# Optimization experiments

Measured on AMD Instinct MI355X. Metric: run time of the kernel, lower is better.

## Reference

```python
import jax, jax.numpy as jnp
import numpy as np

B, L, D = 2, 4096, 2048
H = 8
DK = D // H   # head qk dim = 256
DV = D // H   # head v dim = 256
KCONV = 4
BT = 64       # chunk size
EPS = 1e-5


def setup_inputs() -> dict:
    key = jax.random.key(0)
    ks = jax.random.split(key, 10)
    s = 0.02  # xavier-ish init scale (gain 2**-2.5)
    return {
        "hidden_states": jax.random.normal(ks[0], (B, L, D), jnp.float32),
        "Wq": jax.random.normal(ks[1], (D, D), jnp.float32) * s,
        "Wk": jax.random.normal(ks[2], (D, D), jnp.float32) * s,
        "Wv": jax.random.normal(ks[3], (D, D), jnp.float32) * s,
        "Wb": jax.random.normal(ks[4], (H, D), jnp.float32) * s,
        "conv_q": jax.random.normal(ks[5], (D, KCONV), jnp.float32) * 0.5,
        "conv_k": jax.random.normal(ks[6], (D, KCONV), jnp.float32) * 0.5,
        "conv_v": jax.random.normal(ks[7], (D, KCONV), jnp.float32) * 0.5,
        "g_norm": jnp.ones((DV,), jnp.float32),
        "Wo": jax.random.normal(ks[8], (D, D), jnp.float32) * s,
    }


def _causal_conv_silu(x, w):
    # depthwise causal conv1d (ShortConvolution), x: [B,L,C], w: [C,K]; silu activation
    K = w.shape[1]
    xp = jnp.pad(x, ((0, 0), (K - 1, 0), (0, 0)))
    Lx = x.shape[1]
    y = xp[:, 0:Lx, :] * w[:, 0]
    for j in range(1, K):
        y = y + xp[:, j:j + Lx, :] * w[:, j]
    return jax.nn.silu(y)


def _l2norm(x):
    return x * jax.lax.rsqrt(jnp.sum(x * x, -1, keepdims=True) + 1e-6)


def _chunk_delta_rule(q, k, v, beta):
    # q,k: [B,H,L,DK], v: [B,H,L,DV], beta: [B,H,L]
    b, h, Lq, dk = q.shape
    dv = v.shape[-1]
    nc = Lq // BT
    q = q * (dk ** -0.5)
    kb = k * beta[..., None]
    vb = v * beta[..., None]
    ch = lambda x: x.reshape(b, h, nc, BT, x.shape[-1])
    qc, kc, kbc, vbc = ch(q), ch(k), ch(kb), ch(vb)
    tri_s = jnp.tril(jnp.ones((BT, BT), bool), -1)  # strictly lower
    tri = jnp.tril(jnp.ones((BT, BT), bool))        # lower incl diag
    # M = strict_lower(K_beta K^T); T = (I+M)^{-1} via unit-lower triangular solve
    M = jnp.where(tri_s, jnp.einsum('bhntd,bhnsd->bhnts', kbc, kc), 0.0)
    Lmat = jnp.eye(BT, dtype=q.dtype) + M
    W = jax.scipy.linalg.solve_triangular(Lmat, kbc, lower=True, unit_diagonal=True)  # T @ k_beta
    U = jax.scipy.linalg.solve_triangular(Lmat, vbc, lower=True, unit_diagonal=True)  # T @ v_beta

    def step(S, xs):
        q_i, k_i, w_i, u_i = xs  # each [b,h,BT,d]
        attn = jnp.where(tri, jnp.einsum('bhtd,bhsd->bhts', q_i, k_i), 0.0)
        u_new = u_i - jnp.einsum('bhtd,bhdv->bhtv', w_i, S)
        o_i = jnp.einsum('bhtd,bhdv->bhtv', q_i, S) + jnp.einsum('bhts,bhsv->bhtv', attn, u_new)
        S = S + jnp.einsum('bhtd,bhtv->bhdv', k_i, u_new)
        return S, o_i

    mv = lambda x: jnp.moveaxis(x, 2, 0)  # chunk axis to front for scan
    S0 = jnp.zeros((b, h, dk, dv), q.dtype)
    S, o = jax.lax.scan(step, S0, (mv(qc), mv(kc), mv(W), mv(U)))
    o = jnp.moveaxis(o, 0, 2).reshape(b, h, Lq, dv)
    return o, S


def reference(hidden_states, Wq, Wk, Wv, Wb, conv_q, conv_k, conv_v, g_norm, Wo):
    hs = hidden_states
    q = _causal_conv_silu(hs @ Wq.T, conv_q)
    k = _causal_conv_silu(hs @ Wk.T, conv_k)
    v = _causal_conv_silu(hs @ Wv.T, conv_v)
    tohead = lambda x: x.reshape(B, L, H, -1).transpose(0, 2, 1, 3)  # b l (h d) -> b h l d
    q, k, v = tohead(q), tohead(k), tohead(v)
    q, k = _l2norm(q), _l2norm(k)
    beta = jax.nn.sigmoid(hs @ Wb.T).transpose(0, 2, 1)  # [B,H,L]
    o, _ = _chunk_delta_rule(q, k, v, beta)
    o = o.transpose(0, 2, 1, 3)  # [B,L,H,DV]
    o = o * jax.lax.rsqrt(jnp.mean(o * o, -1, keepdims=True) + EPS) * g_norm  # per-head RMSNorm
    return o.reshape(B, L, D) @ Wo.T
```

## Files before the change

kernel.cpp:

```cpp
#include <hip/hip_runtime.h>
#include <stdint.h>

#define TOK    8192
#define LDIM   4096
#define DDIM   2048
#define NBH    16
#define DK     256
#define NCHUNK 64

typedef __attribute__((ext_vector_type(8))) short bf16x8;
typedef __attribute__((ext_vector_type(4))) float f32x4;

#define MFMA(a,b,c) __builtin_amdgcn_mfma_f32_16x16x32_bf16((a),(b),(c),0,0,0)

__device__ __forceinline__ unsigned short f2bf(float f){
  union { float f; uint32_t u; } v; v.f = f;
  uint32_t r = v.u + 0x7FFFu + ((v.u >> 16) & 1u);
  return (unsigned short)(r >> 16);
}
__device__ __forceinline__ float bf2f(unsigned short u){
  union { uint32_t u; float f; } v; v.u = ((uint32_t)u) << 16;
  return v.f;
}

typedef __attribute__((address_space(1))) unsigned int as1_u32;
typedef __attribute__((address_space(3))) unsigned int as3_u32;
__device__ __forceinline__ void gload16(const void* g, void* l){
  __builtin_amdgcn_global_load_lds((const as1_u32*)g, (as3_u32*)l, 16, 0, 0);
}

__global__ void k_guard(float* o){ if (threadIdx.x == 0) o[0] = 0.f; }

__global__ __launch_bounds__(256) void k_f2bf(const float* __restrict__ s,
                                              unsigned short* __restrict__ d, int n)
{
  int i = (blockIdx.x*256 + threadIdx.x)*4;
  if (i >= n) return;
  float4 v = *(const float4*)(s + i);
  ushort4 o; o.x=f2bf(v.x); o.y=f2bf(v.y); o.z=f2bf(v.z); o.w=f2bf(v.w);
  *(ushort4*)(d + i) = o;
}

__global__ __launch_bounds__(256) void k_beta(const float* __restrict__ hs,
                                              const float* __restrict__ Wb,
                                              float* __restrict__ beta)
{
  const long t = blockIdx.x;
  const int tid = threadIdx.x;
  float acc[8] = {0,0,0,0,0,0,0,0};
  const float* xr = hs + t*DDIM;
  for (int i = tid; i < DDIM; i += 256){
    float x = xr[i];
    #pragma unroll
    for (int h=0; h<8; h++) acc[h] += x * Wb[h*DDIM + i];
  }
  __shared__ float red[8][4];
  const int w = tid >> 6, lane = tid & 63;
  #pragma unroll
  for (int h=0; h<8; h++){
    float s = acc[h];
    #pragma unroll
    for (int off=32; off; off>>=1) s += __shfl_down(s, off, 64);
    if (lane == 0) red[h][w] = s;
  }
  __syncthreads();
  if (tid < 8){
    float s = red[tid][0]+red[tid][1]+red[tid][2]+red[tid][3];
    float bv = 1.f/(1.f + __expf(-s));
    int b = (int)(t >> 12), l = (int)(t & 4095);
    beta[((long)(b*8 + tid))*LDIM + l] = bv;
  }
}

template <bool F32OUT>
__global__ __launch_bounds__(256,2) void k_gemm_bt(
    const unsigned short* __restrict__ A, const unsigned short* __restrict__ Bw,
    void* __restrict__ Cv, int M, int N, int K)
{
  __shared__ unsigned short As[128*32];
  __shared__ unsigned short Bs[128*32];
  const int tid = threadIdx.x;
  const int w = tid >> 6, l = tid & 63;
  const int lo = l & 15, quad = l >> 4;
  const int wm = w >> 1, wn = w & 1;
  const long tm = (long)blockIdx.y * 128, tn = (long)blockIdx.x * 128;
  const int slot0 = (w*2+0)*64 + l;
  const int slot1 = (w*2+1)*64 + l;
  const int r0 = slot0 >> 2, c0 = (slot0 & 3) * 8;
  const int r1 = slot1 >> 2, c1 = (slot1 & 3) * 8;
  const unsigned short* pA0 = A  + (tm + r0)*(long)K + c0;
  const unsigned short* pA1 = A  + (tm + r1)*(long)K + c1;
  const unsigned short* pB0 = Bw + (tn + r0)*(long)K + c0;
  const unsigned short* pB1 = Bw + (tn + r1)*(long)K + c1;
  unsigned short* lA0 = &As[slot0*8]; unsigned short* lA1 = &As[slot1*8];
  unsigned short* lB0 = &Bs[slot0*8]; unsigned short* lB1 = &Bs[slot1*8];
  f32x4 acc[4][4] = {};
  for (int k0 = 0; k0 < K; k0 += 32){
    __syncthreads();
    gload16(pA0 + k0, lA0);
    gload16(pA1 + k0, lA1);
    gload16(pB0 + k0, lB0);
    gload16(pB1 + k0, lB1);
    __syncthreads();
    bf16x8 af[4], bg[4];
    #pragma unroll
    for (int i=0;i<4;i++){
      af[i] = *(const bf16x8*)&As[(wm*64 + i*16 + lo)*32 + quad*8];
      bg[i] = *(const bf16x8*)&Bs[(wn*64 + i*16 + lo)*32 + quad*8];
    }
    #pragma unroll
    for (int mt=0; mt<4; mt++)
      #pragma unroll
      for (int nt=0; nt<4; nt++)
        acc[mt][nt] = MFMA(af[mt], bg[nt], acc[mt][nt]);
  }
  #pragma unroll
  for (int mt=0; mt<4; mt++)
    #pragma unroll
    for (int nt=0; nt<4; nt++)
      #pragma unroll
      for (int r=0; r<4; r++){
        long m = tm + wm*64 + mt*16 + quad*4 + r;
        long n = tn + wn*64 + nt*16 + lo;
        if (F32OUT) ((float*)Cv)[m*N + n] = acc[mt][nt][r];
        else ((unsigned short*)Cv)[m*N + n] = f2bf(acc[mt][nt][r]);
      }
}

__global__ __launch_bounds__(256) void k_conv(
  const unsigned short* __restrict__ X, const float* __restrict__ Wc,
  const float* __restrict__ beta,
  unsigned short* __restrict__ O, int mode)
{
  const int lt = blockIdx.x, bh = blockIdx.y;
  const int b = bh >> 3, h = bh & 7;
  const int d = threadIdx.x;
  const int ch = h*256 + d;
  const int l0 = lt*64;
  const unsigned short* xp = X + (long)b*LDIM*DDIM + ch;
  const float4 wv = *(const float4*)(Wc + ch*4);
  float x0=0.f, x1=0.f, x2=0.f;
  if (l0 >= 3){
    x0 = bf2f(xp[(long)(l0-3)*DDIM]);
    x1 = bf2f(xp[(long)(l0-2)*DDIM]);
    x2 = bf2f(xp[(long)(l0-1)*DDIM]);
  }
  float y[64];
  #pragma unroll
  for (int i=0;i<64;i++){
    float x3 = bf2f(xp[(long)(l0+i)*DDIM]);
    float s = x0*wv.x + x1*wv.y + x2*wv.z + x3*wv.w;
    y[i] = s / (1.f + __expf(-s));
    x0 = x1; x1 = x2; x2 = x3;
  }
  unsigned short* op = O + (long)bh*LDIM*DK + d;
  if (mode == 2){
    const float* bet = beta + (long)bh*LDIM + l0;
    #pragma unroll
    for (int i=0;i<64;i++) op[(long)(l0+i)*DK] = f2bf(y[i]*bet[i]);
    return;
  }
  __shared__ float red[64*4];
  __shared__ float scl[64];
  const int wv_i = threadIdx.x >> 6, lane = threadIdx.x & 63;
  #pragma unroll
  for (int i=0;i<64;i++){
    float ss = y[i]*y[i];
    #pragma unroll
    for (int off=32; off; off>>=1) ss += __shfl_down(ss, off, 64);
    if (lane == 0) red[i*4 + wv_i] = ss;
  }
  __syncthreads();
  if (threadIdx.x < 64){
    int i = threadIdx.x;
    float s = red[i*4]+red[i*4+1]+red[i*4+2]+red[i*4+3];
    scl[i] = rsqrtf(s + 1e-6f) * (mode==0 ? 0.0625f : 1.f);
  }
  __syncthreads();
  #pragma unroll
  for (int i=0;i<64;i++) op[(long)(l0+i)*DK] = f2bf(y[i]*scl[i]);
}

__global__ __launch_bounds__(256) void k_transpose(
  const unsigned short* __restrict__ kH, unsigned short* __restrict__ kT)
{
  const int lt = blockIdx.x, dt = blockIdx.y, bh = blockIdx.z;
  __shared__ unsigned short tk[64][72];
  const int tid = threadIdx.x;
  const int rl = tid >> 2, c0 = (tid & 3) * 16;
  const long base = ((long)bh*LDIM + lt*64 + rl)*DK + dt*64 + c0;
  *(bf16x8*)&tk[rl][c0]   = *(const bf16x8*)(kH + base);
  *(bf16x8*)&tk[rl][c0+8] = *(const bf16x8*)(kH + base + 8);
  __syncthreads();
  const int rd = tid >> 2, lc0 = (tid & 3) * 16;
  bf16x8 ok0, ok1;
  #pragma unroll
  for (int j=0;j<16;j++){
    unsigned short kraw = tk[lc0+j][rd];
    if (j < 8) ok0[j] = (short)kraw; else ok1[j-8] = (short)kraw;
  }
  const long ob = ((long)bh*DK + dt*64 + rd)*LDIM + lt*64 + lc0;
  *(bf16x8*)(kT + ob) = ok0; *(bf16x8*)(kT + ob + 8) = ok1;
}

__global__ __launch_bounds__(256) void k_passA(
  const unsigned short* __restrict__ qH, const unsigned short* __restrict__ kH,
  const unsigned short* vbH,
  const unsigned short* __restrict__ kT,
  const float* __restrict__ beta,
  unsigned short* Wout,
  unsigned short* __restrict__ Uout,
  unsigned short* __restrict__ Aout)
{
  const int c = blockIdx.x, bh = blockIdx.y;
  __shared__ unsigned short Nn[64*72];
  __shared__ unsigned short NT[64*72];
  __shared__ unsigned short Pb[64*72];
  __shared__ unsigned short vT[256*72];
  const int tid = threadIdx.x;
  const int w = tid >> 6, l = tid & 63, lo = l & 15, quad = l >> 4;
  const long tokBase = (long)bh*LDIM + c*64;
  const unsigned short* qrow = qH + tokBase*DK;
  const unsigned short* krow = kH + tokBase*DK;
  const float bv = beta[tokBase + w*16 + lo];

  {
    const int r = tid >> 2, cs = (tid & 3) * 64;
    const unsigned short* vrow = vbH + (tokBase + r)*DK + cs;
    bf16x8 vv[8];
    #pragma unroll
    for (int j=0;j<8;j++) vv[j] = *(const bf16x8*)(vrow + j*8);
    #pragma unroll
    for (int j=0;j<8;j++)
      #pragma unroll
      for (int e=0;e<8;e++)
        vT[(cs + j*8 + e)*72 + r] = (unsigned short)vv[j][e];
  }

  f32x4 mAcc[4] = {}; f32x4 aAcc[4] = {};
  #pragma unroll
  for (int ks=0; ks<8; ks++){
    bf16x8 kf[4];
    #pragma unroll
    for (int nt=0; nt<4; nt++)
      kf[nt] = *(const bf16x8*)&krow[(nt*16+lo)*DK + ks*32 + quad*8];
    bf16x8 qf  = *(const bf16x8*)&qrow[(w*16+lo)*DK + ks*32 + quad*8];
    bf16x8 kfw = *(const bf16x8*)&krow[(w*16+lo)*DK + ks*32 + quad*8];
    bf16x8 kbf;
    #pragma unroll
    for (int j=0;j<8;j++) kbf[j] = (short)f2bf(bf2f((unsigned short)kfw[j]) * bv);
    #pragma unroll
    for (int nt=0; nt<4; nt++){
      mAcc[nt] = MFMA(kbf, kf[nt], mAcc[nt]);
      aAcc[nt] = MFMA(qf,  kf[nt], aAcc[nt]);
    }
  }
  unsigned short* Ap = Aout + ((long)bh*NCHUNK + c)*64*64;
  #pragma unroll
  for (int nt=0; nt<4; nt++)
    #pragma unroll
    for (int r=0; r<4; r++){
      int t = w*16 + quad*4 + r, s = nt*16 + lo;
      float mv = (t > s) ? mAcc[nt][r] : 0.f;
      unsigned short mb = f2bf(mv);
      Nn[t*72+s] = mb;
      NT[s*72+t] = mb;
      Pb[t*72+s] = f2bf((t==s ? 1.f : 0.f) - mv);
      Ap[t*64+s] = f2bf((t >= s) ? aAcc[nt][r] : 0.f);
    }
  __syncthreads();

  #pragma unroll 1
  for (int it=0; it<5; it++){
    bf16x8 aN[2], aP[2], bN[2][4];
    #pragma unroll
    for (int ks=0; ks<2; ks++){
      aN[ks] = *(const bf16x8*)&Nn[(w*16+lo)*72 + ks*32 + quad*8];
      aP[ks] = *(const bf16x8*)&Pb[(w*16+lo)*72 + ks*32 + quad*8];
      #pragma unroll
      for (int nt=0; nt<4; nt++)
        bN[ks][nt] = *(const bf16x8*)&NT[(nt*16+lo)*72 + ks*32 + quad*8];
    }
    f32x4 pp[4];
    #pragma unroll
    for (int nt=0; nt<4; nt++)
      #pragma unroll
      for (int r=0; r<4; r++)
        pp[nt][r] = bf2f(Pb[(w*16+quad*4+r)*72 + nt*16+lo]);
    __syncthreads();
    f32x4 sq[4] = {};
    #pragma unroll
    for (int ks=0; ks<2; ks++)
      #pragma unroll
      for (int nt=0; nt<4; nt++)
        sq[nt] = MFMA(aN[ks], bN[ks][nt], sq[nt]);
    #pragma unroll
    for (int nt=0; nt<4; nt++)
      #pragma unroll
      for (int r=0; r<4; r++){
        int t = w*16 + quad*4 + r, s = nt*16 + lo;
        unsigned short vb2 = f2bf(sq[nt][r]);
        Nn[t*72+s] = vb2; NT[s*72+t] = vb2;
      }
    __syncthreads();
    #pragma unroll
    for (int ks=0; ks<2; ks++)
      #pragma unroll
      for (int nt=0; nt<4; nt++){
        bf16x8 b = *(const bf16x8*)&NT[(nt*16+lo)*72 + ks*32 + quad*8];
        pp[nt] = MFMA(aP[ks], b, pp[nt]);
      }
    #pragma unroll
    for (int nt=0; nt<4; nt++)
      #pragma unroll
      for (int r=0; r<4; r++)
        Pb[(w*16+quad*4+r)*72 + nt*16+lo] = f2bf(pp[nt][r]);
    __syncthreads();
  }

  float b8[2][8];
  #pragma unroll
  for (int ks=0; ks<2; ks++)
    #pragma unroll
    for (int e=0; e<8; e++)
      b8[ks][e] = beta[tokBase + ks*32 + quad*8 + e];
  const unsigned short* kTb = kT + (long)bh*DK*LDIM + c*64;
  unsigned short* Wp = Wout + tokBase*DK;
  unsigned short* Up = Uout + tokBase*DK;
  #pragma unroll 1
  for (int nl=0; nl<4; nl++){
    const int d = (w*4 + nl)*16 + lo;
    f32x4 wa[4] = {}; f32x4 ua[4] = {};
    #pragma unroll
    for (int ks=0; ks<2; ks++){
      bf16x8 braw = *(const bf16x8*)&kTb[(long)d*LDIM + ks*32 + quad*8];
      bf16x8 bw;
      #pragma unroll
      for (int e=0; e<8; e++) bw[e] = (short)f2bf(bf2f((unsigned short)braw[e]) * b8[ks][e]);
      bf16x8 bu = *(const bf16x8*)&vT[d*72 + ks*32 + quad*8];
      #pragma unroll
      for (int mt=0; mt<4; mt++){
        bf16x8 a = *(const bf16x8*)&Pb[(mt*16+lo)*72 + ks*32 + quad*8];
        wa[mt] = MFMA(a, bw, wa[mt]);
        ua[mt] = MFMA(a, bu, ua[mt]);
      }
    }
    #pragma unroll
    for (int mt=0; mt<4; mt++)
      #pragma unroll
      for (int r=0; r<4; r++){
        int t = mt*16 + quad*4 + r;
        Wp[t*DK + d] = f2bf(wa[mt][r]);
        Up[t*DK + d] = f2bf(ua[mt][r]);
      }
  }
}

__device__ __forceinline__ int sidx(int n, int d){
  return n*256 + (((d>>3) ^ (n&7))<<3) + (d&7);
}
__device__ __forceinline__ int uidx(int n, int t){
  return n*64 + ((((t>>3) ^ (n&7)) & 7)<<3) + (t&7);
}

__global__ __launch_bounds__(256) void k_scan(
  const unsigned short* __restrict__ Wm, const unsigned short* __restrict__ Um,
  const unsigned short* __restrict__ qH, const unsigned short* __restrict__ kT,
  const unsigned short* __restrict__ Abuf, unsigned short* __restrict__ oH)
{
  const int bh = blockIdx.x, vb = blockIdx.y;
  __shared__ unsigned short S_l[32*256];
  __shared__ unsigned short u_l[32*64];
  const int tid = threadIdx.x;
  const int w = tid >> 6, l = tid & 63, lo = l & 15, quad = l >> 4;
  for (int i = tid; i < 2048; i += 256) ((unsigned long long*)S_l)[i] = 0ULL;
  f32x4 S[4][2] = {};
  const long hb = (long)bh * LDIM;
  const unsigned short* Wp = Wm + hb*DK;
  const unsigned short* Up = Um + hb*DK;
  const unsigned short* qp = qH + hb*DK;
  const unsigned short* kTp = kT + (long)bh*DK*LDIM;
  const unsigned short* Ap = Abuf + (long)bh*NCHUNK*64*64;
  unsigned short* op = oH + hb*DK;
  __syncthreads();
  #pragma unroll 1
  for (int c = 0; c < NCHUNK; c++){
    const unsigned short* Wc = Wp + (long)c*64*DK;
    const unsigned short* Uc = Up + (long)c*64*DK;
    const unsigned short* qc = qp + (long)c*64*DK;
    const unsigned short* Ac = Ap + (long)c*64*64;
    f32x4 ua[2] = {};
    #pragma unroll
    for (int ks=0; ks<8; ks++){
      bf16x8 a = *(const bf16x8*)&Wc[(w*16+lo)*DK + ks*32 + quad*8];
      #pragma unroll
      for (int nt=0; nt<2; nt++){
        bf16x8 b = *(const bf16x8*)&S_l[sidx(nt*16+lo, ks*32+quad*8)];
        ua[nt] = MFMA(a, b, ua[nt]);
      }
    }
    #pragma unroll
    for (int nt=0; nt<2; nt++){
      int n = nt*16 + lo;
      int t0 = w*16 + quad*4;
      ushort4 pk;
      pk.x = f2bf(bf2f(Uc[(t0+0)*DK + vb*32 + n]) - ua[nt][0]);
      pk.y = f2bf(bf2f(Uc[(t0+1)*DK + vb*32 + n]) - ua[nt][1]);
      pk.z = f2bf(bf2f(Uc[(t0+2)*DK + vb*32 + n]) - ua[nt][2]);
      pk.w = f2bf(bf2f(Uc[(t0+3)*DK + vb*32 + n]) - ua[nt][3]);
      *(ushort4*)&u_l[uidx(n, t0)] = pk;
    }
    __syncthreads();
    f32x4 oa[2] = {};
    #pragma unroll
    for (int ks=0; ks<8; ks++){
      bf16x8 a = *(const bf16x8*)&qc[(w*16+lo)*DK + ks*32 + quad*8];
      #pragma unroll
      for (int nt=0; nt<2; nt++){
        bf16x8 b = *(const bf16x8*)&S_l[sidx(nt*16+lo, ks*32+quad*8)];
        oa[nt] = MFMA(a, b, oa[nt]);
      }
    }
    #pragma unroll
    for (int ks=0; ks<2; ks++){
      bf16x8 a = *(const bf16x8*)&Ac[(w*16+lo)*64 + ks*32 + quad*8];
      #pragma unroll
      for (int nt=0; nt<2; nt++){
        bf16x8 b = *(const bf16x8*)&u_l[uidx(nt*16+lo, ks*32+quad*8)];
        oa[nt] = MFMA(a, b, oa[nt]);
      }
    }
    #pragma unroll
    for (int nt=0; nt<2; nt++)
      #pragma unroll
      for (int r=0; r<4; r++)
        op[(long)(c*64 + w*16 + quad*4 + r)*DK + vb*32 + nt*16 + lo] = f2bf(oa[nt][r]);
    #pragma unroll
    for (int mtl=0; mtl<4; mtl++){
      int drow = w*64 + mtl*16 + lo;
      #pragma unroll
      for (int ks=0; ks<2; ks++){
        bf16x8 a = *(const bf16x8*)&kTp[(long)drow*LDIM + c*64 + ks*32 + quad*8];
        #pragma unroll
        for (int nt=0; nt<2; nt++){
          bf16x8 b = *(const bf16x8*)&u_l[uidx(nt*16+lo, ks*32+quad*8)];
          S[mtl][nt] = MFMA(a, b, S[mtl][nt]);
        }
      }
    }
    __syncthreads();
    #pragma unroll
    for (int mtl=0; mtl<4; mtl++)
      #pragma unroll
      for (int nt=0; nt<2; nt++){
        int n = nt*16 + lo;
        int d0 = w*64 + mtl*16 + quad*4;
        ushort4 pk;
        pk.x = f2bf(S[mtl][nt][0]); pk.y = f2bf(S[mtl][nt][1]);
        pk.z = f2bf(S[mtl][nt][2]); pk.w = f2bf(S[mtl][nt][3]);
        *(ushort4*)&S_l[sidx(n, d0)] = pk;
      }
    __syncthreads();
  }
}

__global__ __launch_bounds__(64) void k_rms(
  const unsigned short* __restrict__ oH, const float* __restrict__ g,
  unsigned short* __restrict__ oN)
{
  const int ln = blockIdx.x, bh = blockIdx.y;
  const int b = bh >> 3, h = bh & 7;
  ushort4 u = *(const ushort4*)(oH + ((long)bh*LDIM + ln)*DK + threadIdx.x*4);
  float4 v; v.x = bf2f(u.x); v.y = bf2f(u.y); v.z = bf2f(u.z); v.w = bf2f(u.w);
  float ss = v.x*v.x + v.y*v.y + v.z*v.z + v.w*v.w;
  #pragma unroll
  for (int off=32; off; off>>=1) ss += __shfl_down(ss, off, 64);
  ss = __shfl(ss, 0, 64);
  const float sc = rsqrtf(ss*(1.f/DK) + 1e-5f);
  const float4 gv = *(const float4*)(g + threadIdx.x*4);
  unsigned short* o = oN + ((long)b*LDIM + ln)*DDIM + h*DK + threadIdx.x*4;
  ushort4 pk; pk.x=f2bf(v.x*sc*gv.x); pk.y=f2bf(v.y*sc*gv.y);
  pk.z=f2bf(v.z*sc*gv.z); pk.w=f2bf(v.w*sc*gv.w);
  *(ushort4*)o = pk;
}

extern "C" void kernel_launch(void* const* d_in, const int* in_sizes, int n_in,
                              void* d_out, int out_size, void* d_ws, size_t ws_size,
                              hipStream_t stream)
{
  (void)in_sizes; (void)n_in; (void)out_size;
  const float* hs = (const float*)d_in[0];
  const float* Wq = (const float*)d_in[1];
  const float* Wk = (const float*)d_in[2];
  const float* Wv = (const float*)d_in[3];
  const float* Wb = (const float*)d_in[4];
  const float* cq = (const float*)d_in[5];
  const float* ck = (const float*)d_in[6];
  const float* cv = (const float*)d_in[7];
  const float* gn = (const float*)d_in[8];
  const float* Wo = (const float*)d_in[9];

  const size_t SZ_TD2 = (size_t)TOK*DDIM*2;
  const size_t SZ_DD2 = (size_t)DDIM*DDIM*2;
  const size_t NEED  = 5*SZ_TD2 + 2*SZ_DD2 + (size_t)NBH*LDIM*4;
  const size_t NEEDW = NEED + SZ_TD2;
  if (ws_size < NEED){ k_guard<<<1, 64, 0, stream>>>((float*)d_out); return; }

  char* p = (char*)d_ws;
  unsigned short* bufA = (unsigned short*)p;      p += SZ_TD2;
  unsigned short* bufB = (unsigned short*)p;      p += SZ_DD2;
  unsigned short* bufC = (unsigned short*)p;      p += SZ_TD2;
  unsigned short* bufD = (unsigned short*)p;      p += SZ_TD2;
  unsigned short* bufE = (unsigned short*)p;      p += SZ_TD2;
  unsigned short* bufF = (unsigned short*)p;      p += SZ_TD2;
  unsigned short* bufG = (unsigned short*)p;      p += SZ_DD2;
  float*          beta = (float*)p;               p += (size_t)NBH*LDIM*4;
  unsigned short* bufW = (ws_size >= NEEDW) ? (unsigned short*)p : bufF;

  const dim3 gg(DDIM/128, TOK/128);
  const dim3 cg(LDIM/64, NBH);
  const int nTD = TOK*DDIM, nDD = DDIM*DDIM;

  k_f2bf<<<dim3(nTD/1024), 256, 0, stream>>>(hs, bufA, nTD);
  k_beta<<<dim3(TOK), 256, 0, stream>>>(hs, Wb, beta);

  k_f2bf<<<dim3(nDD/1024), 256, 0, stream>>>(Wq, bufB, nDD);
  k_gemm_bt<false><<<gg, 256, 0, stream>>>(bufA, bufB, bufC, TOK, DDIM, DDIM);
  k_conv<<<cg, 256, 0, stream>>>(bufC, cq, beta, bufD, 0);

  k_f2bf<<<dim3(nDD/1024), 256, 0, stream>>>(Wk, bufB, nDD);
  k_gemm_bt<false><<<gg, 256, 0, stream>>>(bufA, bufB, bufC, TOK, DDIM, DDIM);
  k_conv<<<cg, 256, 0, stream>>>(bufC, ck, beta, bufE, 1);

  k_f2bf<<<dim3(nDD/1024), 256, 0, stream>>>(Wv, bufB, nDD);
  k_gemm_bt<false><<<gg, 256, 0, stream>>>(bufA, bufB, bufC, TOK, DDIM, DDIM);
  k_conv<<<cg, 256, 0, stream>>>(bufC, cv, beta, bufF, 2);

  k_transpose<<<dim3(LDIM/64, DK/64, NBH), 256, 0, stream>>>(bufE, bufC);
  k_passA<<<dim3(NCHUNK, NBH), 256, 0, stream>>>(bufD, bufE, bufF, bufC, beta,
                                                 bufW, bufA , bufG);
  k_scan<<<dim3(NBH, 8), 256, 0, stream>>>(bufW, bufA, bufD, bufC, bufG, bufE);
  k_rms<<<dim3(LDIM, NBH), 64, 0, stream>>>(bufE, gn, bufC);

  k_f2bf<<<dim3(nDD/1024), 256, 0, stream>>>(Wo, bufB, nDD);
  k_gemm_bt<true><<<gg, 256, 0, stream>>>(bufC, bufB, d_out , TOK, DDIM, DDIM);
}
```

Baseline: 1.028 ms.

## Prefetch next chunk's W/U into registers in scan and swizzle GEMM tile order

The sequential chunk scan kernel now loads the next chunk's W and U operands into registers one chunk ahead, using a two-buffer ping-pong with the loop unrolled by two. It also issues the q, A and kT loads for the current chunk before the first MFMA so global latency is hidden on the serial critical path, and sets launch bounds to one block per CU to leave room for the extra registers. Separately, the GEMM remaps workgroup IDs in groups of eight, likely to improve L2 locality or spread tiles across XCDs. The costs are higher register pressure in the scan and a redundant load of the last chunk on the final iteration.

```diff
diff --git a/kernel.cpp b/kernel.cpp
--- a/kernel.cpp
+++ b/kernel.cpp
@@ -83,7 +83,15 @@
   const int w = tid >> 6, l = tid & 63;
   const int lo = l & 15, quad = l >> 4;
   const int wm = w >> 1, wn = w & 1;
-  const long tm = (long)blockIdx.y * 128, tn = (long)blockIdx.x * 128;
+  const int gx = gridDim.x;
+  int id = blockIdx.y * gx + blockIdx.x;
+  const int nwg = gx * gridDim.y;
+  if ((nwg & 7) == 0){
+    const int q8 = nwg >> 3;
+    id = (id & 7) * q8 + (id >> 3);
+  }
+  const int bx = id % gx, by = id / gx;
+  const long tm = (long)by * 128, tn = (long)bx * 128;
   const int slot0 = (w*2+0)*64 + l;
   const int slot1 = (w*2+1)*64 + l;
   const int r0 = slot0 >> 2, c0 = (slot0 & 3) * 8;
@@ -363,7 +371,116 @@
   return n*64 + ((((t>>3) ^ (n&7)) & 7)<<3) + (t&7);
 }
 
-__global__ __launch_bounds__(256) void k_scan(
+struct PrefWU {
+  bf16x8 wf[8];
+  unsigned short uf[8];
+};
+
+__device__ __forceinline__ void load_wu(PrefWU& P,
+    const unsigned short* __restrict__ Wp, const unsigned short* __restrict__ Up,
+    int c, int w, int lo, int quad, int vb)
+{
+  const unsigned short* Wc = Wp + (long)c*64*DK;
+  const unsigned short* Uc = Up + (long)c*64*DK;
+  #pragma unroll
+  for (int ks=0; ks<8; ks++)
+    P.wf[ks] = *(const bf16x8*)&Wc[(w*16+lo)*DK + ks*32 + quad*8];
+  const int t0 = w*16 + quad*4;
+  #pragma unroll
+  for (int nt=0; nt<2; nt++)
+    #pragma unroll
+    for (int r=0; r<4; r++)
+      P.uf[nt*4+r] = Uc[(t0+r)*DK + vb*32 + nt*16 + lo];
+}
+
+__device__ __forceinline__ void scan_chunk(const PrefWU& P, int c,
+  const unsigned short* __restrict__ qp, const unsigned short* __restrict__ kTp,
+  const unsigned short* __restrict__ Ap, unsigned short* __restrict__ op,
+  unsigned short* S_l, unsigned short* u_l, f32x4 (&S)[4][2],
+  int w, int lo, int quad, int vb)
+{
+  const unsigned short* qc = qp + (long)c*64*DK;
+  const unsigned short* Ac = Ap + (long)c*64*64;
+  bf16x8 qf[8], af[2], kf[4][2];
+  #pragma unroll
+  for (int ks=0; ks<8; ks++)
+    qf[ks] = *(const bf16x8*)&qc[(w*16+lo)*DK + ks*32 + quad*8];
+  #pragma unroll
+  for (int ks=0; ks<2; ks++)
+    af[ks] = *(const bf16x8*)&Ac[(w*16+lo)*64 + ks*32 + quad*8];
+  #pragma unroll
+  for (int mtl=0; mtl<4; mtl++)
+    #pragma unroll
+    for (int ks=0; ks<2; ks++)
+      kf[mtl][ks] = *(const bf16x8*)&kTp[(long)(w*64+mtl*16+lo)*LDIM + c*64 + ks*32 + quad*8];
+
+  f32x4 ua[2] = {};
+  #pragma unroll
+  for (int ks=0; ks<8; ks++)
+    #pragma unroll
+    for (int nt=0; nt<2; nt++){
+      bf16x8 b = *(const bf16x8*)&S_l[sidx(nt*16+lo, ks*32+quad*8)];
+      ua[nt] = MFMA(P.wf[ks], b, ua[nt]);
+    }
+  {
+    const int t0 = w*16 + quad*4;
+    #pragma unroll
+    for (int nt=0; nt<2; nt++){
+      const int n = nt*16 + lo;
+      ushort4 pk;
+      pk.x = f2bf(bf2f(P.uf[nt*4+0]) - ua[nt][0]);
+      pk.y = f2bf(bf2f(P.uf[nt*4+1]) - ua[nt][1]);
+      pk.z = f2bf(bf2f(P.uf[nt*4+2]) - ua[nt][2]);
+      pk.w = f2bf(bf2f(P.uf[nt*4+3]) - ua[nt][3]);
+      *(ushort4*)&u_l[uidx(n, t0)] = pk;
+    }
+  }
+  __syncthreads();
+  f32x4 oa[2] = {};
+  #pragma unroll
+  for (int ks=0; ks<8; ks++)
+    #pragma unroll
+    for (int nt=0; nt<2; nt++){
+      bf16x8 b = *(const bf16x8*)&S_l[sidx(nt*16+lo, ks*32+quad*8)];
+      oa[nt] = MFMA(qf[ks], b, oa[nt]);
+    }
+  #pragma unroll
+  for (int ks=0; ks<2; ks++)
+    #pragma unroll
+    for (int nt=0; nt<2; nt++){
+      bf16x8 b = *(const bf16x8*)&u_l[uidx(nt*16+lo, ks*32+quad*8)];
+      oa[nt] = MFMA(af[ks], b, oa[nt]);
+    }
+  #pragma unroll
+  for (int nt=0; nt<2; nt++)
+    #pragma unroll
+    for (int r=0; r<4; r++)
+      op[(long)(c*64 + w*16 + quad*4 + r)*DK + vb*32 + nt*16 + lo] = f2bf(oa[nt][r]);
+  #pragma unroll
+  for (int mtl=0; mtl<4; mtl++)
+    #pragma unroll
+    for (int ks=0; ks<2; ks++)
+      #pragma unroll
+      for (int nt=0; nt<2; nt++){
+        bf16x8 b = *(const bf16x8*)&u_l[uidx(nt*16+lo, ks*32+quad*8)];
+        S[mtl][nt] = MFMA(kf[mtl][ks], b, S[mtl][nt]);
+      }
+  __syncthreads();
+  #pragma unroll
+  for (int mtl=0; mtl<4; mtl++)
+    #pragma unroll
+    for (int nt=0; nt<2; nt++){
+      const int n = nt*16 + lo;
+      const int d0 = w*64 + mtl*16 + quad*4;
+      ushort4 pk;
+      pk.x = f2bf(S[mtl][nt][0]); pk.y = f2bf(S[mtl][nt][1]);
+      pk.z = f2bf(S[mtl][nt][2]); pk.w = f2bf(S[mtl][nt][3]);
+      *(ushort4*)&S_l[sidx(n, d0)] = pk;
+    }
+  __syncthreads();
+}
+
+__global__ __launch_bounds__(256,1) void k_scan(
   const unsigned short* __restrict__ Wm, const unsigned short* __restrict__ Um,
   const unsigned short* __restrict__ qH, const unsigned short* __restrict__ kT,
   const unsigned short* __restrict__ Abuf, unsigned short* __restrict__ oH)
@@ -382,85 +499,15 @@
   const unsigned short* kTp = kT + (long)bh*DK*LDIM;
   const unsigned short* Ap = Abuf + (long)bh*NCHUNK*64*64;
   unsigned short* op = oH + hb*DK;
+  PrefWU PA, PB;
+  load_wu(PA, Wp, Up, 0, w, lo, quad, vb);
   __syncthreads();
   #pragma unroll 1
-  for (int c = 0; c < NCHUNK; c++){
-    const unsigned short* Wc = Wp + (long)c*64*DK;
-    const unsigned short* Uc = Up + (long)c*64*DK;
-    const unsigned short* qc = qp + (long)c*64*DK;
-    const unsigned short* Ac = Ap + (long)c*64*64;
-    f32x4 ua[2] = {};
-    #pragma unroll
-    for (int ks=0; ks<8; ks++){
-      bf16x8 a = *(const bf16x8*)&Wc[(w*16+lo)*DK + ks*32 + quad*8];
-      #pragma unroll
-      for (int nt=0; nt<2; nt++){
-        bf16x8 b = *(const bf16x8*)&S_l[sidx(nt*16+lo, ks*32+quad*8)];
-        ua[nt] = MFMA(a, b, ua[nt]);
-      }
-    }
-    #pragma unroll
-    for (int nt=0; nt<2; nt++){
-      int n = nt*16 + lo;
-      int t0 = w*16 + quad*4;
-      ushort4 pk;
-      pk.x = f2bf(bf2f(Uc[(t0+0)*DK + vb*32 + n]) - ua[nt][0]);
-      pk.y = f2bf(bf2f(Uc[(t0+1)*DK + vb*32 + n]) - ua[nt][1]);
-      pk.z = f2bf(bf2f(Uc[(t0+2)*DK + vb*32 + n]) - ua[nt][2]);
-      pk.w = f2bf(bf2f(Uc[(t0+3)*DK + vb*32 + n]) - ua[nt][3]);
-      *(ushort4*)&u_l[uidx(n, t0)] = pk;
-    }
-    __syncthreads();
-    f32x4 oa[2] = {};
-    #pragma unroll
-    for (int ks=0; ks<8; ks++){
-      bf16x8 a = *(const bf16x8*)&qc[(w*16+lo)*DK + ks*32 + quad*8];
-      #pragma unroll
-      for (int nt=0; nt<2; nt++){
-        bf16x8 b = *(const bf16x8*)&S_l[sidx(nt*16+lo, ks*32+quad*8)];
-        oa[nt] = MFMA(a, b, oa[nt]);
-      }
-    }
-    #pragma unroll
-    for (int ks=0; ks<2; ks++){
-      bf16x8 a = *(const bf16x8*)&Ac[(w*16+lo)*64 + ks*32 + quad*8];
-      #pragma unroll
-      for (int nt=0; nt<2; nt++){
-        bf16x8 b = *(const bf16x8*)&u_l[uidx(nt*16+lo, ks*32+quad*8)];
-        oa[nt] = MFMA(a, b, oa[nt]);
-      }
-    }
-    #pragma unroll
-    for (int nt=0; nt<2; nt++)
-      #pragma unroll
-      for (int r=0; r<4; r++)
-        op[(long)(c*64 + w*16 + quad*4 + r)*DK + vb*32 + nt*16 + lo] = f2bf(oa[nt][r]);
-    #pragma unroll
-    for (int mtl=0; mtl<4; mtl++){
-      int drow = w*64 + mtl*16 + lo;
-      #pragma unroll
-      for (int ks=0; ks<2; ks++){
-        bf16x8 a = *(const bf16x8*)&kTp[(long)drow*LDIM + c*64 + ks*32 + quad*8];
-        #pragma unroll
-        for (int nt=0; nt<2; nt++){
-          bf16x8 b = *(const bf16x8*)&u_l[uidx(nt*16+lo, ks*32+quad*8)];
-          S[mtl][nt] = MFMA(a, b, S[mtl][nt]);
-        }
-      }
-    }
-    __syncthreads();
-    #pragma unroll
-    for (int mtl=0; mtl<4; mtl++)
-      #pragma unroll
-      for (int nt=0; nt<2; nt++){
-        int n = nt*16 + lo;
-        int d0 = w*64 + mtl*16 + quad*4;
-        ushort4 pk;
-        pk.x = f2bf(S[mtl][nt][0]); pk.y = f2bf(S[mtl][nt][1]);
-        pk.z = f2bf(S[mtl][nt][2]); pk.w = f2bf(S[mtl][nt][3]);
-        *(ushort4*)&S_l[sidx(n, d0)] = pk;
-      }
-    __syncthreads();
+  for (int c = 0; c < NCHUNK; c += 2){
+    load_wu(PB, Wp, Up, c+1, w, lo, quad, vb);
+    scan_chunk(PA, c,   qp, kTp, Ap, op, S_l, u_l, S, w, lo, quad, vb);
+    load_wu(PA, Wp, Up, (c+2 < NCHUNK) ? c+2 : NCHUNK-1, w, lo, quad, vb);
+    scan_chunk(PB, c+1, qp, kTp, Ap, op, S_l, u_l, S, w, lo, quad, vb);
   }
 }
 
```

New measurement: 956.4 us. 1.07x faster.
